# Kernel optimization log

Measured on AMD Instinct MI355X. Metric: run time of the kernel, lower is better.

## Reference

```python
import jax, jax.numpy as jnp
import numpy as np

BN_EPS = 1e-5


def setup_inputs() -> dict:
    key = jax.random.key(0)
    ks = jax.random.split(key, 4)
    N, V, C = 64, 512, 512
    K, OUT = 2, 512
    x = jax.random.normal(ks[0], (N, V, C), dtype=jnp.float32)
    A = jax.random.uniform(ks[1], (N, K, V, V), dtype=jnp.float32) / V
    conv_w = jax.random.normal(ks[2], (2 * OUT, C), dtype=jnp.float32) / np.sqrt(C)
    conv_b = jax.random.normal(ks[3], (2 * OUT,), dtype=jnp.float32) * 0.01
    gamma = jnp.ones((2 * OUT,), dtype=jnp.float32)
    beta = jnp.zeros((2 * OUT,), dtype=jnp.float32)
    eps_p = jnp.zeros((1,), dtype=jnp.float32)
    return {"x": x, "A": A, "conv_w": conv_w, "conv_b": conv_b,
            "gamma": gamma, "beta": beta, "eps_p": eps_p}


def reference(x, A, conv_w, conv_b, gamma, beta, eps_p):
    # x: (N, V, C); A: (N, K, V, V)
    N, V, C = x.shape
    K = A.shape[1]
    # 1x1 Conv1d over nodes: (N, 2*out, V)
    h = jnp.einsum('nvc,oc->nov', x, conv_w) + conv_b[None, :, None]
    # BatchNorm1d, training-mode batch stats (biased variance, per channel)
    mean = jnp.mean(h, axis=(0, 2), keepdims=True)
    var = jnp.var(h, axis=(0, 2), keepdims=True)
    h = (h - mean) * jax.lax.rsqrt(var + BN_EPS) * gamma[None, :, None] + beta[None, :, None]
    c2 = h.shape[1]
    h = h.reshape(N, K, c2 // K, V)  # (N, K, out, V)
    # graph propagation: x A then (x A) A^T, contracted over node dims
    t = jnp.einsum('nkcm,nkme->nkce', h, A)
    At = jnp.transpose(A, (0, 1, 3, 2))
    y = jnp.einsum('nkce,nkem->ncm', t, At)  # (N, out, V)
    out = (1.0 + eps_p[0]) * x + jnp.transpose(y, (0, 2, 1))
    return out, At
```

## Files before the change

### kernel.cpp

```cpp
#include <hip/hip_runtime.h>
#include <stdint.h>

typedef __bf16 bf16x8 __attribute__((ext_vector_type(8)));
typedef float f32x4 __attribute__((ext_vector_type(4)));
typedef unsigned short us4_t __attribute__((ext_vector_type(4)));
typedef unsigned short us8_t __attribute__((ext_vector_type(8)));

#define LDSK 40

__device__ __forceinline__ unsigned short f2bf(float f) {
  __bf16 b = (__bf16)f;
  return __builtin_bit_cast(unsigned short, b);
}
__device__ __forceinline__ float bf2f(unsigned short u) {
  union { uint32_t u; float f; } v; v.u = ((uint32_t)u) << 16;
  return v.f;
}

__device__ __forceinline__ void gload16(const void* g, void* l) {
  __builtin_amdgcn_global_load_lds(
      (const __attribute__((address_space(1))) void*)g,
      (__attribute__((address_space(3))) void*)l, 16, 0, 0);
}

__device__ __forceinline__ void stage_tile(const unsigned short* g, size_t ldg,
                                           unsigned short* lds, int wid, int lane) {
#pragma unroll
  for (int i = 0; i < 2; ++i) {
    int seg = wid * 2 + i;
    const unsigned short* gp = g + (size_t)(seg * 16 + (lane >> 2)) * ldg + (lane & 3) * 8;
    gload16(gp, lds + seg * 512);
  }
}

__device__ __forceinline__ void mfma_step(const unsigned short* As, const unsigned short* Bs,
                                          int ldb, f32x4 (*acc)[4],
                                          int wr, int wc, int lr, int lk) {
  bf16x8 a[4], b[4];
#pragma unroll
  for (int mi = 0; mi < 4; ++mi)
    a[mi] = *(const bf16x8*)(As + (wr + mi * 16 + lr) * 32 + lk * 8);
#pragma unroll
  for (int ni = 0; ni < 4; ++ni)
    b[ni] = *(const bf16x8*)(Bs + (wc + ni * 16 + lr) * ldb + lk * 8);
#pragma unroll
  for (int mi = 0; mi < 4; ++mi)
#pragma unroll
    for (int ni = 0; ni < 4; ++ni)
      acc[mi][ni] = __builtin_amdgcn_mfma_f32_16x16x32_bf16(a[mi], b[ni], acc[mi][ni], 0, 0, 0);
}

__global__ __launch_bounds__(256) void k_convert(
    const float* __restrict__ X, const float* __restrict__ W,
    unsigned short* __restrict__ Xb, unsigned short* __restrict__ Wb) {
  const size_t idx = (size_t)blockIdx.x * 256 + threadIdx.x;
  const size_t stride = (size_t)gridDim.x * 256;
  for (size_t i = idx; i < (size_t)16777216 / 8; i += stride) {
    float4 f0 = ((const float4*)X)[2 * i], f1 = ((const float4*)X)[2 * i + 1];
    us8_t w = { f2bf(f0.x), f2bf(f0.y), f2bf(f0.z), f2bf(f0.w),
                f2bf(f1.x), f2bf(f1.y), f2bf(f1.z), f2bf(f1.w) };
    ((us8_t*)Xb)[i] = w;
  }
  for (size_t i = idx; i < (size_t)524288 / 8; i += stride) {
    float4 f0 = ((const float4*)W)[2 * i], f1 = ((const float4*)W)[2 * i + 1];
    us8_t w = { f2bf(f0.x), f2bf(f0.y), f2bf(f0.z), f2bf(f0.w),
                f2bf(f1.x), f2bf(f1.y), f2bf(f1.z), f2bf(f1.w) };
    ((us8_t*)Wb)[i] = w;
  }
}

__global__ __launch_bounds__(256) void k_gemm1(
    const unsigned short* __restrict__ Wb, const unsigned short* __restrict__ Xb,
    const float* __restrict__ convb, unsigned short* __restrict__ H) {
  __shared__ unsigned short As[4096];
  __shared__ unsigned short Bs[4096];
  const int tid = threadIdx.x;
  const int L = blockIdx.x;
  const int xcd = L & 7, slot = L >> 3;
  const int n = xcd * 8 + (slot >> 5);
  const int tile = slot & 31;
  const int tm = tile >> 2, tn = tile & 3;
  const unsigned short* gA = Wb + (size_t)tm * 128 * 512;
  const unsigned short* gB = Xb + ((size_t)n * 512 + tn * 128) * 512;
  const int lane = tid & 63, wid = tid >> 6;
  const int wr = (wid >> 1) * 64, wc = (wid & 1) * 64;
  const int lr = lane & 15, lk = lane >> 4;
  f32x4 acc[4][4] = {};
  for (int k0 = 0; k0 < 512; k0 += 32) {
    stage_tile(gA + k0, 512, As, wid, lane);
    stage_tile(gB + k0, 512, Bs, wid, lane);
    __syncthreads();
    mfma_step(As, Bs, 32, acc, wr, wc, lr, lk);
    __syncthreads();
  }
  unsigned short* Hn = H + (size_t)n * 1024 * 512;
#pragma unroll
  for (int mi = 0; mi < 4; ++mi)
#pragma unroll
    for (int i = 0; i < 4; ++i) {
      int o = tm * 128 + wr + mi * 16 + lk * 4 + i;
      float bias = convb[o];
#pragma unroll
      for (int ni = 0; ni < 4; ++ni) {
        int v = tn * 128 + wc + ni * 16 + lr;
        Hn[(size_t)o * 512 + v] = f2bf(acc[mi][ni][i] + bias);
      }
    }
}

__global__ __launch_bounds__(256) void k_bn_at_ab(
    const unsigned short* __restrict__ H, const float* __restrict__ gamma,
    const float* __restrict__ beta, float* __restrict__ sc_sh,
    const float* __restrict__ A, float* __restrict__ At,
    unsigned short* __restrict__ Ab) {
  const int tid = threadIdx.x;
  if (blockIdx.x < 1024) {
    const int o = blockIdx.x;
    const int g = tid >> 6, l = tid & 63;
    float s1 = 0.f, s2 = 0.f;
    for (int step = 0; step < 16; ++step) {
      int n = g + step * 4;
      const us8_t* row = (const us8_t*)(H + ((size_t)n * 1024 + o) * 512);
      us8_t v = row[l];
#pragma unroll
      for (int j = 0; j < 8; ++j) { float f = bf2f(v[j]); s1 += f; s2 += f * f; }
    }
    __shared__ float r1[256], r2[256];
    r1[tid] = s1; r2[tid] = s2;
    __syncthreads();
    for (int off = 128; off > 0; off >>= 1) {
      if (tid < off) { r1[tid] += r1[tid + off]; r2[tid] += r2[tid + off]; }
      __syncthreads();
    }
    if (tid == 0) {
      float mean = r1[0] * (1.0f / 32768.0f);
      float var = r2[0] * (1.0f / 32768.0f) - mean * mean;
      float s = gamma[o] * rsqrtf(var + 1e-5f);
      sc_sh[o] = s;
      sc_sh[1024 + o] = beta[o] - mean * s;
    }
  } else {
    __shared__ float tile[64][65];
    const int tIdx = blockIdx.x - 1024;
    const int nk = tIdx >> 6;
    const int e0 = (tIdx & 7) * 64, m0 = ((tIdx >> 3) & 7) * 64;
    const float* src = A + (size_t)nk * 262144;
    float* dst = At + (size_t)nk * 262144;
    unsigned short* ab = Ab + (size_t)nk * 262144;
#pragma unroll
    for (int j = 0; j < 4; ++j) {
      int ch = tid + j * 256;
      int r = ch >> 4, c4 = (ch & 15) * 4;
      float4 f = *(const float4*)(src + (size_t)(m0 + r) * 512 + e0 + c4);
      tile[r][c4] = f.x; tile[r][c4 + 1] = f.y; tile[r][c4 + 2] = f.z; tile[r][c4 + 3] = f.w;
      us4_t u = { f2bf(f.x), f2bf(f.y), f2bf(f.z), f2bf(f.w) };
      *(us4_t*)(ab + (size_t)(m0 + r) * 512 + e0 + c4) = u;
    }
    __syncthreads();
#pragma unroll
    for (int j = 0; j < 4; ++j) {
      int ch = tid + j * 256;
      int e = ch >> 4, m4 = (ch & 15) * 4;
      float4 g = { tile[m4][e], tile[m4 + 1][e], tile[m4 + 2][e], tile[m4 + 3][e] };
      *(float4*)(dst + (size_t)(e0 + e) * 512 + m0 + m4) = g;
    }
  }
}

__global__ __launch_bounds__(256) void k_bn_convA(
    const unsigned short* __restrict__ H, const float* __restrict__ gamma,
    const float* __restrict__ beta, float* __restrict__ sc_sh,
    const float* __restrict__ A, unsigned short* __restrict__ Ab) {
  const int tid = threadIdx.x;
  if (blockIdx.x < 1024) {
    const int o = blockIdx.x;
    const int g = tid >> 6, l = tid & 63;
    float s1 = 0.f, s2 = 0.f;
    for (int step = 0; step < 16; ++step) {
      int n = g + step * 4;
      const us8_t* row = (const us8_t*)(H + ((size_t)n * 1024 + o) * 512);
      us8_t v = row[l];
#pragma unroll
      for (int j = 0; j < 8; ++j) { float f = bf2f(v[j]); s1 += f; s2 += f * f; }
    }
    __shared__ float r1[256], r2[256];
    r1[tid] = s1; r2[tid] = s2;
    __syncthreads();
    for (int off = 128; off > 0; off >>= 1) {
      if (tid < off) { r1[tid] += r1[tid + off]; r2[tid] += r2[tid + off]; }
      __syncthreads();
    }
    if (tid == 0) {
      float mean = r1[0] * (1.0f / 32768.0f);
      float var = r2[0] * (1.0f / 32768.0f) - mean * mean;
      float s = gamma[o] * rsqrtf(var + 1e-5f);
      sc_sh[o] = s;
      sc_sh[1024 + o] = beta[o] - mean * s;
    }
  } else {
    const size_t idx = (size_t)(blockIdx.x - 1024) * 256 + tid;
    const size_t stride = (size_t)2048 * 256;
    for (size_t i = idx; i < (size_t)33554432 / 8; i += stride) {
      float4 f0 = ((const float4*)A)[2 * i], f1 = ((const float4*)A)[2 * i + 1];
      us8_t w = { f2bf(f0.x), f2bf(f0.y), f2bf(f0.z), f2bf(f0.w),
                  f2bf(f1.x), f2bf(f1.y), f2bf(f1.z), f2bf(f1.w) };
      ((us8_t*)Ab)[i] = w;
    }
  }
}

__global__ __launch_bounds__(256) void k_bn(
    const unsigned short* __restrict__ H, const float* __restrict__ gamma,
    const float* __restrict__ beta, float* __restrict__ sc_sh) {
  const int o = blockIdx.x;
  const int tid = threadIdx.x;
  const int g = tid >> 6, l = tid & 63;
  float s1 = 0.f, s2 = 0.f;
  for (int step = 0; step < 16; ++step) {
    int n = g + step * 4;
    const us8_t* row = (const us8_t*)(H + ((size_t)n * 1024 + o) * 512);
    us8_t v = row[l];
#pragma unroll
    for (int j = 0; j < 8; ++j) { float f = bf2f(v[j]); s1 += f; s2 += f * f; }
  }
  __shared__ float r1[256], r2[256];
  r1[tid] = s1; r2[tid] = s2;
  __syncthreads();
  for (int off = 128; off > 0; off >>= 1) {
    if (tid < off) { r1[tid] += r1[tid + off]; r2[tid] += r2[tid + off]; }
    __syncthreads();
  }
  if (tid == 0) {
    float mean = r1[0] * (1.0f / 32768.0f);
    float var = r2[0] * (1.0f / 32768.0f) - mean * mean;
    float s = gamma[o] * rsqrtf(var + 1e-5f);
    sc_sh[o] = s;
    sc_sh[1024 + o] = beta[o] - mean * s;
  }
}

__global__ __launch_bounds__(256) void k_convertA(
    const float* __restrict__ A, unsigned short* __restrict__ Ab) {
  const size_t idx = (size_t)blockIdx.x * 256 + threadIdx.x;
  const size_t stride = (size_t)gridDim.x * 256;
  for (size_t i = idx; i < (size_t)33554432 / 8; i += stride) {
    float4 f0 = ((const float4*)A)[2 * i], f1 = ((const float4*)A)[2 * i + 1];
    us8_t w = { f2bf(f0.x), f2bf(f0.y), f2bf(f0.z), f2bf(f0.w),
                f2bf(f1.x), f2bf(f1.y), f2bf(f1.z), f2bf(f1.w) };
    ((us8_t*)Ab)[i] = w;
  }
}

__global__ __launch_bounds__(256) void k_affine(
    unsigned short* __restrict__ H, const float* __restrict__ sc_sh) {
  const size_t idx = (size_t)blockIdx.x * 256 + threadIdx.x;
  const size_t stride = (size_t)gridDim.x * 256;
  const size_t total8 = (size_t)64 * 1024 * 512 / 8;
  for (size_t i = idx; i < total8; i += stride) {
    size_t base = i * 8;
    int o = (int)((base >> 9) & 1023);
    float sc = sc_sh[o], sh = sc_sh[1024 + o];
    us8_t v = ((const us8_t*)H)[i];
    us8_t w;
#pragma unroll
    for (int j = 0; j < 8; ++j) w[j] = f2bf(fmaf(bf2f(v[j]), sc, sh));
    ((us8_t*)H)[i] = w;
  }
}

__global__ __launch_bounds__(256) void k_aat(
    const unsigned short* __restrict__ Ab, unsigned short* __restrict__ B2) {
  __shared__ unsigned short As[4096];
  __shared__ unsigned short Bs[4096];
  const int tid = threadIdx.x;
  const int L = blockIdx.x;
  const int xcd = L & 7, slot = L >> 3;
  const int nk = xcd * 16 + (slot >> 4);
  const int tile = slot & 15;
  const int tm = tile >> 2, tn = tile & 3;
  const unsigned short* Ank = Ab + (size_t)nk * 262144;
  const unsigned short* gA = Ank + (size_t)tm * 128 * 512;
  const unsigned short* gB = Ank + (size_t)tn * 128 * 512;
  const int lane = tid & 63, wid = tid >> 6;
  const int wr = (wid >> 1) * 64, wc = (wid & 1) * 64;
  const int lr = lane & 15, lk = lane >> 4;
  f32x4 acc[4][4] = {};
  for (int k0 = 0; k0 < 512; k0 += 32) {
    stage_tile(gA + k0, 512, As, wid, lane);
    stage_tile(gB + k0, 512, Bs, wid, lane);
    __syncthreads();
    mfma_step(As, Bs, 32, acc, wr, wc, lr, lk);
    __syncthreads();
  }
  unsigned short* Bn = B2 + (size_t)nk * 262144;
#pragma unroll
  for (int mi = 0; mi < 4; ++mi)
#pragma unroll
    for (int i = 0; i < 4; ++i) {
      int m = tm * 128 + wr + mi * 16 + lk * 4 + i;
#pragma unroll
      for (int ni = 0; ni < 4; ++ni) {
        int mp = tn * 128 + wc + ni * 16 + lr;
        Bn[(size_t)m * 512 + mp] = f2bf(acc[mi][ni][i]);
      }
    }
}

template <bool AFFINE>
__global__ __launch_bounds__(256) void k_gemm3(
    const unsigned short* __restrict__ B2, const unsigned short* __restrict__ H,
    const float* __restrict__ sc_sh, const float* __restrict__ X,
    const float* __restrict__ epsp, float* __restrict__ out) {
  __shared__ unsigned short As[4096];
  __shared__ unsigned short Bs[128 * LDSK];
  __shared__ float s_sc[2][128], s_sh[2][128];
  const int tid = threadIdx.x;
  const int L = blockIdx.x;
  const int xcd = L & 7, slot = L >> 3;
  const int n = xcd * 8 + (slot >> 4);
  const int tile = slot & 15;
  const int tm = tile >> 2, tn = tile & 3;
  const int lane = tid & 63, wid = tid >> 6;
  const int wr = (wid >> 1) * 64, wc = (wid & 1) * 64;
  const int lr = lane & 15, lk = lane >> 4;
  if (AFFINE) {
    if (tid < 256) {
      int kkq = tid >> 7, r = tid & 127;
      s_sc[kkq][r] = sc_sh[kkq * 512 + tn * 128 + r];
      s_sh[kkq][r] = sc_sh[1024 + kkq * 512 + tn * 128 + r];
    }
    __syncthreads();
  }
  f32x4 acc[4][4] = {};
  for (int kk = 0; kk < 2; ++kk) {
    const unsigned short* gA = B2 + ((size_t)(n * 2 + kk) * 512 + tm * 128) * 512;
    const unsigned short* gB = H + ((size_t)n * 1024 + kk * 512 + tn * 128) * 512;
    for (int k0 = 0; k0 < 512; k0 += 32) {
      stage_tile(gA + k0, 512, As, wid, lane);
#pragma unroll
      for (int i = 0; i < 2; ++i) {
        int s = tid + i * 256;
        int r = s >> 2, c8 = (s & 3) * 8;
        us8_t v = *(const us8_t*)(gB + (size_t)r * 512 + k0 + c8);
        if (AFFINE) {
          float sc = s_sc[kk][r], sh = s_sh[kk][r];
          us8_t w;
#pragma unroll
          for (int j = 0; j < 8; ++j) w[j] = f2bf(fmaf(bf2f(v[j]), sc, sh));
          *(us8_t*)&Bs[r * LDSK + c8] = w;
        } else {
          *(us8_t*)&Bs[r * LDSK + c8] = v;
        }
      }
      __syncthreads();
      mfma_step(As, Bs, LDSK, acc, wr, wc, lr, lk);
      __syncthreads();
    }
  }
  const float e1 = 1.0f + epsp[0];
#pragma unroll
  for (int mi = 0; mi < 4; ++mi)
#pragma unroll
    for (int i = 0; i < 4; ++i) {
      int v = tm * 128 + wr + mi * 16 + lk * 4 + i;
#pragma unroll
      for (int ni = 0; ni < 4; ++ni) {
        int c = tn * 128 + wc + ni * 16 + lr;
        size_t idx = ((size_t)n * 512 + v) * 512 + c;
        out[idx] = fmaf(e1, X[idx], acc[mi][ni][i]);
      }
    }
}

__global__ __launch_bounds__(256) void k_at(
    const float* __restrict__ A, float* __restrict__ At) {
  __shared__ float tile[64][65];
  const int nk = blockIdx.z;
  const int e0 = blockIdx.x * 64, m0 = blockIdx.y * 64;
  const float* src = A + (size_t)nk * 262144;
  float* dst = At + (size_t)nk * 262144;
  const int t = threadIdx.x;
#pragma unroll
  for (int j = 0; j < 4; ++j) {
    int ch = t + j * 256;
    int r = ch >> 4, c4 = (ch & 15) * 4;
    float4 f = *(const float4*)(src + (size_t)(m0 + r) * 512 + e0 + c4);
    tile[r][c4] = f.x; tile[r][c4 + 1] = f.y; tile[r][c4 + 2] = f.z; tile[r][c4 + 3] = f.w;
  }
  __syncthreads();
#pragma unroll
  for (int j = 0; j < 4; ++j) {
    int ch = t + j * 256;
    int e = ch >> 4, m4 = (ch & 15) * 4;
    float4 g = { tile[m4][e], tile[m4 + 1][e], tile[m4 + 2][e], tile[m4 + 3][e] };
    *(float4*)(dst + (size_t)(e0 + e) * 512 + m0 + m4) = g;
  }
}

extern "C" void kernel_launch(void* const* d_in, const int* in_sizes, int n_in,
                              void* d_out, int out_size, void* d_ws, size_t ws_size,
                              hipStream_t stream) {
  const float* x      = (const float*)d_in[0];
  const float* A      = (const float*)d_in[1];
  const float* conv_w = (const float*)d_in[2];
  const float* conv_b = (const float*)d_in[3];
  const float* gamma  = (const float*)d_in[4];
  const float* beta   = (const float*)d_in[5];
  const float* eps_p  = (const float*)d_in[6];

  float* out = (float*)d_out;
  float* At  = out + (size_t)16777216;

  unsigned short* Xb = (unsigned short*)out;
  unsigned short* Wb = Xb + (size_t)16777216;
  unsigned short* Ab = (unsigned short*)out;

  const size_t WS_BIG = (size_t)2 * 67108864 + 8192;
  if (ws_size >= WS_BIG) {
    unsigned short* H  = (unsigned short*)d_ws;
    unsigned short* B2 = H + (size_t)33554432;
    float* sc_sh = (float*)(B2 + (size_t)33554432);
    k_convert    <<<2048, 256, 0, stream>>>(x, conv_w, Xb, Wb);
    k_gemm1      <<<2048, 256, 0, stream>>>(Wb, Xb, conv_b, H);
    k_bn_at_ab   <<<9216, 256, 0, stream>>>(H, gamma, beta, sc_sh, A, At, Ab);
    k_aat        <<<2048, 256, 0, stream>>>(Ab, B2);
    k_gemm3<true><<<1024, 256, 0, stream>>>(B2, H, sc_sh, x, eps_p, out);
    return;
  }

  unsigned short* B2 = (unsigned short*)At;
  unsigned short* H  = (unsigned short*)(At + (size_t)16777216);
  float* wsf = (float*)d_ws;

  if (ws_size >= 8192) {
    float* sc_sh = wsf;
    k_convert    <<<2048, 256, 0, stream>>>(x, conv_w, Xb, Wb);
    k_gemm1      <<<2048, 256, 0, stream>>>(Wb, Xb, conv_b, H);
    k_bn_convA   <<<3072, 256, 0, stream>>>(H, gamma, beta, sc_sh, A, Ab);
    k_aat        <<<2048, 256, 0, stream>>>(Ab, B2);
    k_gemm3<true><<<1024, 256, 0, stream>>>(B2, H, sc_sh, x, eps_p, out);
  } else {
    float* sc_sh = out;
    k_convert     <<<2048, 256, 0, stream>>>(x, conv_w, Xb, Wb);
    k_gemm1       <<<2048, 256, 0, stream>>>(Wb, Xb, conv_b, H);
    k_bn          <<<1024, 256, 0, stream>>>(H, gamma, beta, sc_sh);
    k_affine      <<<2048, 256, 0, stream>>>(H, sc_sh);
    k_convertA    <<<2048, 256, 0, stream>>>(A, Ab);
    k_aat         <<<2048, 256, 0, stream>>>(Ab, B2);
    k_gemm3<false><<<1024, 256, 0, stream>>>(B2, H, nullptr, x, eps_p, out);
  }
  k_at<<<dim3(8, 8, 128), 256, 0, stream>>>(A, At);
}
```

Measured before the change: 276.7 us.

## Add large-workspace path fusing A transpose/convert with X convert and BN with AAT

```diff
diff --git a/kernel.cpp b/kernel.cpp
--- a/kernel.cpp
+++ b/kernel.cpp
@@ -50,98 +50,43 @@
       acc[mi][ni] = __builtin_amdgcn_mfma_f32_16x16x32_bf16(a[mi], b[ni], acc[mi][ni], 0, 0, 0);
 }
 
-__global__ __launch_bounds__(256) void k_convert(
-    const float* __restrict__ X, const float* __restrict__ W,
-    unsigned short* __restrict__ Xb, unsigned short* __restrict__ Wb) {
-  const size_t idx = (size_t)blockIdx.x * 256 + threadIdx.x;
-  const size_t stride = (size_t)gridDim.x * 256;
-  for (size_t i = idx; i < (size_t)16777216 / 8; i += stride) {
-    float4 f0 = ((const float4*)X)[2 * i], f1 = ((const float4*)X)[2 * i + 1];
-    us8_t w = { f2bf(f0.x), f2bf(f0.y), f2bf(f0.z), f2bf(f0.w),
-                f2bf(f1.x), f2bf(f1.y), f2bf(f1.z), f2bf(f1.w) };
-    ((us8_t*)Xb)[i] = w;
-  }
-  for (size_t i = idx; i < (size_t)524288 / 8; i += stride) {
-    float4 f0 = ((const float4*)W)[2 * i], f1 = ((const float4*)W)[2 * i + 1];
-    us8_t w = { f2bf(f0.x), f2bf(f0.y), f2bf(f0.z), f2bf(f0.w),
-                f2bf(f1.x), f2bf(f1.y), f2bf(f1.z), f2bf(f1.w) };
-    ((us8_t*)Wb)[i] = w;
-  }
-}
-
-__global__ __launch_bounds__(256) void k_gemm1(
-    const unsigned short* __restrict__ Wb, const unsigned short* __restrict__ Xb,
-    const float* __restrict__ convb, unsigned short* __restrict__ H) {
-  __shared__ unsigned short As[4096];
-  __shared__ unsigned short Bs[4096];
-  const int tid = threadIdx.x;
-  const int L = blockIdx.x;
-  const int xcd = L & 7, slot = L >> 3;
-  const int n = xcd * 8 + (slot >> 5);
-  const int tile = slot & 31;
-  const int tm = tile >> 2, tn = tile & 3;
-  const unsigned short* gA = Wb + (size_t)tm * 128 * 512;
-  const unsigned short* gB = Xb + ((size_t)n * 512 + tn * 128) * 512;
-  const int lane = tid & 63, wid = tid >> 6;
-  const int wr = (wid >> 1) * 64, wc = (wid & 1) * 64;
-  const int lr = lane & 15, lk = lane >> 4;
-  f32x4 acc[4][4] = {};
-  for (int k0 = 0; k0 < 512; k0 += 32) {
-    stage_tile(gA + k0, 512, As, wid, lane);
-    stage_tile(gB + k0, 512, Bs, wid, lane);
-    __syncthreads();
-    mfma_step(As, Bs, 32, acc, wr, wc, lr, lk);
-    __syncthreads();
-  }
-  unsigned short* Hn = H + (size_t)n * 1024 * 512;
-#pragma unroll
-  for (int mi = 0; mi < 4; ++mi)
-#pragma unroll
-    for (int i = 0; i < 4; ++i) {
-      int o = tm * 128 + wr + mi * 16 + lk * 4 + i;
-      float bias = convb[o];
-#pragma unroll
-      for (int ni = 0; ni < 4; ++ni) {
-        int v = tn * 128 + wc + ni * 16 + lr;
-        Hn[(size_t)o * 512 + v] = f2bf(acc[mi][ni][i] + bias);
-      }
-    }
-}
-
-__global__ __launch_bounds__(256) void k_bn_at_ab(
+__device__ __forceinline__ void bn_block(
     const unsigned short* __restrict__ H, const float* __restrict__ gamma,
     const float* __restrict__ beta, float* __restrict__ sc_sh,
-    const float* __restrict__ A, float* __restrict__ At,
+    int o, int tid, float* r1, float* r2) {
+  const int g = tid >> 6, l = tid & 63;
+  float s1 = 0.f, s2 = 0.f;
+  for (int step = 0; step < 16; ++step) {
+    int n = g + step * 4;
+    const us8_t* row = (const us8_t*)(H + ((size_t)n * 1024 + o) * 512);
+    us8_t v = row[l];
+#pragma unroll
+    for (int j = 0; j < 8; ++j) { float f = bf2f(v[j]); s1 += f; s2 += f * f; }
+  }
+  r1[tid] = s1; r2[tid] = s2;
+  __syncthreads();
+  for (int off = 128; off > 0; off >>= 1) {
+    if (tid < off) { r1[tid] += r1[tid + off]; r2[tid] += r2[tid + off]; }
+    __syncthreads();
+  }
+  if (tid == 0) {
+    float mean = r1[0] * (1.0f / 32768.0f);
+    float var = r2[0] * (1.0f / 32768.0f) - mean * mean;
+    float s = gamma[o] * rsqrtf(var + 1e-5f);
+    sc_sh[o] = s;
+    sc_sh[1024 + o] = beta[o] - mean * s;
+  }
+}
+
+__global__ __launch_bounds__(256) void k_convert_all(
+    const float* __restrict__ X, const float* __restrict__ W,
+    const float* __restrict__ A, unsigned short* __restrict__ Xb,
+    unsigned short* __restrict__ Wb, float* __restrict__ At,
     unsigned short* __restrict__ Ab) {
   const int tid = threadIdx.x;
-  if (blockIdx.x < 1024) {
-    const int o = blockIdx.x;
-    const int g = tid >> 6, l = tid & 63;
-    float s1 = 0.f, s2 = 0.f;
-    for (int step = 0; step < 16; ++step) {
-      int n = g + step * 4;
-      const us8_t* row = (const us8_t*)(H + ((size_t)n * 1024 + o) * 512);
-      us8_t v = row[l];
-#pragma unroll
-      for (int j = 0; j < 8; ++j) { float f = bf2f(v[j]); s1 += f; s2 += f * f; }
-    }
-    __shared__ float r1[256], r2[256];
-    r1[tid] = s1; r2[tid] = s2;
-    __syncthreads();
-    for (int off = 128; off > 0; off >>= 1) {
-      if (tid < off) { r1[tid] += r1[tid + off]; r2[tid] += r2[tid + off]; }
-      __syncthreads();
-    }
-    if (tid == 0) {
-      float mean = r1[0] * (1.0f / 32768.0f);
-      float var = r2[0] * (1.0f / 32768.0f) - mean * mean;
-      float s = gamma[o] * rsqrtf(var + 1e-5f);
-      sc_sh[o] = s;
-      sc_sh[1024 + o] = beta[o] - mean * s;
-    }
-  } else {
+  if (blockIdx.x < 8192) {
     __shared__ float tile[64][65];
-    const int tIdx = blockIdx.x - 1024;
+    const int tIdx = blockIdx.x;
     const int nk = tIdx >> 6;
     const int e0 = (tIdx & 7) * 64, m0 = ((tIdx >> 3) & 7) * 64;
     const float* src = A + (size_t)nk * 262144;
@@ -164,115 +109,35 @@
       float4 g = { tile[m4][e], tile[m4 + 1][e], tile[m4 + 2][e], tile[m4 + 3][e] };
       *(float4*)(dst + (size_t)(e0 + e) * 512 + m0 + m4) = g;
     }
-  }
-}
-
-__global__ __launch_bounds__(256) void k_bn_convA(
-    const unsigned short* __restrict__ H, const float* __restrict__ gamma,
-    const float* __restrict__ beta, float* __restrict__ sc_sh,
-    const float* __restrict__ A, unsigned short* __restrict__ Ab) {
-  const int tid = threadIdx.x;
-  if (blockIdx.x < 1024) {
-    const int o = blockIdx.x;
-    const int g = tid >> 6, l = tid & 63;
-    float s1 = 0.f, s2 = 0.f;
-    for (int step = 0; step < 16; ++step) {
-      int n = g + step * 4;
-      const us8_t* row = (const us8_t*)(H + ((size_t)n * 1024 + o) * 512);
-      us8_t v = row[l];
-#pragma unroll
-      for (int j = 0; j < 8; ++j) { float f = bf2f(v[j]); s1 += f; s2 += f * f; }
-    }
-    __shared__ float r1[256], r2[256];
-    r1[tid] = s1; r2[tid] = s2;
-    __syncthreads();
-    for (int off = 128; off > 0; off >>= 1) {
-      if (tid < off) { r1[tid] += r1[tid + off]; r2[tid] += r2[tid + off]; }
-      __syncthreads();
-    }
-    if (tid == 0) {
-      float mean = r1[0] * (1.0f / 32768.0f);
-      float var = r2[0] * (1.0f / 32768.0f) - mean * mean;
-      float s = gamma[o] * rsqrtf(var + 1e-5f);
-      sc_sh[o] = s;
-      sc_sh[1024 + o] = beta[o] - mean * s;
-    }
   } else {
-    const size_t idx = (size_t)(blockIdx.x - 1024) * 256 + tid;
+    const size_t idx = (size_t)(blockIdx.x - 8192) * 256 + tid;
     const size_t stride = (size_t)2048 * 256;
-    for (size_t i = idx; i < (size_t)33554432 / 8; i += stride) {
-      float4 f0 = ((const float4*)A)[2 * i], f1 = ((const float4*)A)[2 * i + 1];
+    for (size_t i = idx; i < (size_t)16777216 / 8; i += stride) {
+      float4 f0 = ((const float4*)X)[2 * i], f1 = ((const float4*)X)[2 * i + 1];
       us8_t w = { f2bf(f0.x), f2bf(f0.y), f2bf(f0.z), f2bf(f0.w),
                   f2bf(f1.x), f2bf(f1.y), f2bf(f1.z), f2bf(f1.w) };
-      ((us8_t*)Ab)[i] = w;
-    }
-  }
-}
-
-__global__ __launch_bounds__(256) void k_bn(
+      ((us8_t*)Xb)[i] = w;
+    }
+    for (size_t i = idx; i < (size_t)524288 / 8; i += stride) {
+      float4 f0 = ((const float4*)W)[2 * i], f1 = ((const float4*)W)[2 * i + 1];
+      us8_t w = { f2bf(f0.x), f2bf(f0.y), f2bf(f0.z), f2bf(f0.w),
+                  f2bf(f1.x), f2bf(f1.y), f2bf(f1.z), f2bf(f1.w) };
+      ((us8_t*)Wb)[i] = w;
+    }
+  }
+}
+
+__global__ __launch_bounds__(256) void k_aat_bn(
+    const unsigned short* __restrict__ Ab, unsigned short* __restrict__ B2,
     const unsigned short* __restrict__ H, const float* __restrict__ gamma,
     const float* __restrict__ beta, float* __restrict__ sc_sh) {
-  const int o = blockIdx.x;
-  const int tid = threadIdx.x;
-  const int g = tid >> 6, l = tid & 63;
-  float s1 = 0.f, s2 = 0.f;
-  for (int step = 0; step < 16; ++step) {
-    int n = g + step * 4;
-    const us8_t* row = (const us8_t*)(H + ((size_t)n * 1024 + o) * 512);
-    us8_t v = row[l];
-#pragma unroll
-    for (int j = 0; j < 8; ++j) { float f = bf2f(v[j]); s1 += f; s2 += f * f; }
-  }
-  __shared__ float r1[256], r2[256];
-  r1[tid] = s1; r2[tid] = s2;
-  __syncthreads();
-  for (int off = 128; off > 0; off >>= 1) {
-    if (tid < off) { r1[tid] += r1[tid + off]; r2[tid] += r2[tid + off]; }
-    __syncthreads();
-  }
-  if (tid == 0) {
-    float mean = r1[0] * (1.0f / 32768.0f);
-    float var = r2[0] * (1.0f / 32768.0f) - mean * mean;
-    float s = gamma[o] * rsqrtf(var + 1e-5f);
-    sc_sh[o] = s;
-    sc_sh[1024 + o] = beta[o] - mean * s;
-  }
-}
-
-__global__ __launch_bounds__(256) void k_convertA(
-    const float* __restrict__ A, unsigned short* __restrict__ Ab) {
-  const size_t idx = (size_t)blockIdx.x * 256 + threadIdx.x;
-  const size_t stride = (size_t)gridDim.x * 256;
-  for (size_t i = idx; i < (size_t)33554432 / 8; i += stride) {
-    float4 f0 = ((const float4*)A)[2 * i], f1 = ((const float4*)A)[2 * i + 1];
-    us8_t w = { f2bf(f0.x), f2bf(f0.y), f2bf(f0.z), f2bf(f0.w),
-                f2bf(f1.x), f2bf(f1.y), f2bf(f1.z), f2bf(f1.w) };
-    ((us8_t*)Ab)[i] = w;
-  }
-}
-
-__global__ __launch_bounds__(256) void k_affine(
-    unsigned short* __restrict__ H, const float* __restrict__ sc_sh) {
-  const size_t idx = (size_t)blockIdx.x * 256 + threadIdx.x;
-  const size_t stride = (size_t)gridDim.x * 256;
-  const size_t total8 = (size_t)64 * 1024 * 512 / 8;
-  for (size_t i = idx; i < total8; i += stride) {
-    size_t base = i * 8;
-    int o = (int)((base >> 9) & 1023);
-    float sc = sc_sh[o], sh = sc_sh[1024 + o];
-    us8_t v = ((const us8_t*)H)[i];
-    us8_t w;
-#pragma unroll
-    for (int j = 0; j < 8; ++j) w[j] = f2bf(fmaf(bf2f(v[j]), sc, sh));
-    ((us8_t*)H)[i] = w;
-  }
-}
-
-__global__ __launch_bounds__(256) void k_aat(
-    const unsigned short* __restrict__ Ab, unsigned short* __restrict__ B2) {
   __shared__ unsigned short As[4096];
   __shared__ unsigned short Bs[4096];
   const int tid = threadIdx.x;
+  if (blockIdx.x >= 2048) {
+    bn_block(H, gamma, beta, sc_sh, blockIdx.x - 2048, tid, (float*)As, (float*)Bs);
+    return;
+  }
   const int L = blockIdx.x;
   const int xcd = L & 7, slot = L >> 3;
   const int nk = xcd * 16 + (slot >> 4);
@@ -306,6 +171,195 @@
     }
 }
 
+__global__ __launch_bounds__(256) void k_convert(
+    const float* __restrict__ X, const float* __restrict__ W,
+    unsigned short* __restrict__ Xb, unsigned short* __restrict__ Wb) {
+  const size_t idx = (size_t)blockIdx.x * 256 + threadIdx.x;
+  const size_t stride = (size_t)gridDim.x * 256;
+  for (size_t i = idx; i < (size_t)16777216 / 8; i += stride) {
+    float4 f0 = ((const float4*)X)[2 * i], f1 = ((const float4*)X)[2 * i + 1];
+    us8_t w = { f2bf(f0.x), f2bf(f0.y), f2bf(f0.z), f2bf(f0.w),
+                f2bf(f1.x), f2bf(f1.y), f2bf(f1.z), f2bf(f1.w) };
+    ((us8_t*)Xb)[i] = w;
+  }
+  for (size_t i = idx; i < (size_t)524288 / 8; i += stride) {
+    float4 f0 = ((const float4*)W)[2 * i], f1 = ((const float4*)W)[2 * i + 1];
+    us8_t w = { f2bf(f0.x), f2bf(f0.y), f2bf(f0.z), f2bf(f0.w),
+                f2bf(f1.x), f2bf(f1.y), f2bf(f1.z), f2bf(f1.w) };
+    ((us8_t*)Wb)[i] = w;
+  }
+}
+
+__global__ __launch_bounds__(256) void k_gemm1(
+    const unsigned short* __restrict__ Wb, const unsigned short* __restrict__ Xb,
+    const float* __restrict__ convb, unsigned short* __restrict__ H) {
+  __shared__ unsigned short As[4096];
+  __shared__ unsigned short Bs[4096];
+  const int tid = threadIdx.x;
+  const int L = blockIdx.x;
+  const int xcd = L & 7, slot = L >> 3;
+  const int n = xcd * 8 + (slot >> 5);
+  const int tile = slot & 31;
+  const int tm = tile >> 2, tn = tile & 3;
+  const unsigned short* gA = Wb + (size_t)tm * 128 * 512;
+  const unsigned short* gB = Xb + ((size_t)n * 512 + tn * 128) * 512;
+  const int lane = tid & 63, wid = tid >> 6;
+  const int wr = (wid >> 1) * 64, wc = (wid & 1) * 64;
+  const int lr = lane & 15, lk = lane >> 4;
+  f32x4 acc[4][4] = {};
+  for (int k0 = 0; k0 < 512; k0 += 32) {
+    stage_tile(gA + k0, 512, As, wid, lane);
+    stage_tile(gB + k0, 512, Bs, wid, lane);
+    __syncthreads();
+    mfma_step(As, Bs, 32, acc, wr, wc, lr, lk);
+    __syncthreads();
+  }
+  unsigned short* Hn = H + (size_t)n * 1024 * 512;
+#pragma unroll
+  for (int mi = 0; mi < 4; ++mi)
+#pragma unroll
+    for (int i = 0; i < 4; ++i) {
+      int o = tm * 128 + wr + mi * 16 + lk * 4 + i;
+      float bias = convb[o];
+#pragma unroll
+      for (int ni = 0; ni < 4; ++ni) {
+        int v = tn * 128 + wc + ni * 16 + lr;
+        Hn[(size_t)o * 512 + v] = f2bf(acc[mi][ni][i] + bias);
+      }
+    }
+}
+
+__global__ __launch_bounds__(256) void k_bn_at_ab(
+    const unsigned short* __restrict__ H, const float* __restrict__ gamma,
+    const float* __restrict__ beta, float* __restrict__ sc_sh,
+    const float* __restrict__ A, float* __restrict__ At,
+    unsigned short* __restrict__ Ab) {
+  const int tid = threadIdx.x;
+  if (blockIdx.x < 1024) {
+    __shared__ float r1[256], r2[256];
+    bn_block(H, gamma, beta, sc_sh, blockIdx.x, tid, r1, r2);
+  } else {
+    __shared__ float tile[64][65];
+    const int tIdx = blockIdx.x - 1024;
+    const int nk = tIdx >> 6;
+    const int e0 = (tIdx & 7) * 64, m0 = ((tIdx >> 3) & 7) * 64;
+    const float* src = A + (size_t)nk * 262144;
+    float* dst = At + (size_t)nk * 262144;
+    unsigned short* ab = Ab + (size_t)nk * 262144;
+#pragma unroll
+    for (int j = 0; j < 4; ++j) {
+      int ch = tid + j * 256;
+      int r = ch >> 4, c4 = (ch & 15) * 4;
+      float4 f = *(const float4*)(src + (size_t)(m0 + r) * 512 + e0 + c4);
+      tile[r][c4] = f.x; tile[r][c4 + 1] = f.y; tile[r][c4 + 2] = f.z; tile[r][c4 + 3] = f.w;
+      us4_t u = { f2bf(f.x), f2bf(f.y), f2bf(f.z), f2bf(f.w) };
+      *(us4_t*)(ab + (size_t)(m0 + r) * 512 + e0 + c4) = u;
+    }
+    __syncthreads();
+#pragma unroll
+    for (int j = 0; j < 4; ++j) {
+      int ch = tid + j * 256;
+      int e = ch >> 4, m4 = (ch & 15) * 4;
+      float4 g = { tile[m4][e], tile[m4 + 1][e], tile[m4 + 2][e], tile[m4 + 3][e] };
+      *(float4*)(dst + (size_t)(e0 + e) * 512 + m0 + m4) = g;
+    }
+  }
+}
+
+__global__ __launch_bounds__(256) void k_bn_convA(
+    const unsigned short* __restrict__ H, const float* __restrict__ gamma,
+    const float* __restrict__ beta, float* __restrict__ sc_sh,
+    const float* __restrict__ A, unsigned short* __restrict__ Ab) {
+  const int tid = threadIdx.x;
+  if (blockIdx.x < 1024) {
+    __shared__ float r1[256], r2[256];
+    bn_block(H, gamma, beta, sc_sh, blockIdx.x, tid, r1, r2);
+  } else {
+    const size_t idx = (size_t)(blockIdx.x - 1024) * 256 + tid;
+    const size_t stride = (size_t)2048 * 256;
+    for (size_t i = idx; i < (size_t)33554432 / 8; i += stride) {
+      float4 f0 = ((const float4*)A)[2 * i], f1 = ((const float4*)A)[2 * i + 1];
+      us8_t w = { f2bf(f0.x), f2bf(f0.y), f2bf(f0.z), f2bf(f0.w),
+                  f2bf(f1.x), f2bf(f1.y), f2bf(f1.z), f2bf(f1.w) };
+      ((us8_t*)Ab)[i] = w;
+    }
+  }
+}
+
+__global__ __launch_bounds__(256) void k_bn(
+    const unsigned short* __restrict__ H, const float* __restrict__ gamma,
+    const float* __restrict__ beta, float* __restrict__ sc_sh) {
+  __shared__ float r1[256], r2[256];
+  bn_block(H, gamma, beta, sc_sh, blockIdx.x, threadIdx.x, r1, r2);
+}
+
+__global__ __launch_bounds__(256) void k_convertA(
+    const float* __restrict__ A, unsigned short* __restrict__ Ab) {
+  const size_t idx = (size_t)blockIdx.x * 256 + threadIdx.x;
+  const size_t stride = (size_t)gridDim.x * 256;
+  for (size_t i = idx; i < (size_t)33554432 / 8; i += stride) {
+    float4 f0 = ((const float4*)A)[2 * i], f1 = ((const float4*)A)[2 * i + 1];
+    us8_t w = { f2bf(f0.x), f2bf(f0.y), f2bf(f0.z), f2bf(f0.w),
+                f2bf(f1.x), f2bf(f1.y), f2bf(f1.z), f2bf(f1.w) };
+    ((us8_t*)Ab)[i] = w;
+  }
+}
+
+__global__ __launch_bounds__(256) void k_affine(
+    unsigned short* __restrict__ H, const float* __restrict__ sc_sh) {
+  const size_t idx = (size_t)blockIdx.x * 256 + threadIdx.x;
+  const size_t stride = (size_t)gridDim.x * 256;
+  const size_t total8 = (size_t)64 * 1024 * 512 / 8;
+  for (size_t i = idx; i < total8; i += stride) {
+    size_t base = i * 8;
+    int o = (int)((base >> 9) & 1023);
+    float sc = sc_sh[o], sh = sc_sh[1024 + o];
+    us8_t v = ((const us8_t*)H)[i];
+    us8_t w;
+#pragma unroll
+    for (int j = 0; j < 8; ++j) w[j] = f2bf(fmaf(bf2f(v[j]), sc, sh));
+    ((us8_t*)H)[i] = w;
+  }
+}
+
+__global__ __launch_bounds__(256) void k_aat(
+    const unsigned short* __restrict__ Ab, unsigned short* __restrict__ B2) {
+  __shared__ unsigned short As[4096];
+  __shared__ unsigned short Bs[4096];
+  const int tid = threadIdx.x;
+  const int L = blockIdx.x;
+  const int xcd = L & 7, slot = L >> 3;
+  const int nk = xcd * 16 + (slot >> 4);
+  const int tile = slot & 15;
+  const int tm = tile >> 2, tn = tile & 3;
+  const unsigned short* Ank = Ab + (size_t)nk * 262144;
+  const unsigned short* gA = Ank + (size_t)tm * 128 * 512;
+  const unsigned short* gB = Ank + (size_t)tn * 128 * 512;
+  const int lane = tid & 63, wid = tid >> 6;
+  const int wr = (wid >> 1) * 64, wc = (wid & 1) * 64;
+  const int lr = lane & 15, lk = lane >> 4;
+  f32x4 acc[4][4] = {};
+  for (int k0 = 0; k0 < 512; k0 += 32) {
+    stage_tile(gA + k0, 512, As, wid, lane);
+    stage_tile(gB + k0, 512, Bs, wid, lane);
+    __syncthreads();
+    mfma_step(As, Bs, 32, acc, wr, wc, lr, lk);
+    __syncthreads();
+  }
+  unsigned short* Bn = B2 + (size_t)nk * 262144;
+#pragma unroll
+  for (int mi = 0; mi < 4; ++mi)
+#pragma unroll
+    for (int i = 0; i < 4; ++i) {
+      int m = tm * 128 + wr + mi * 16 + lk * 4 + i;
+#pragma unroll
+      for (int ni = 0; ni < 4; ++ni) {
+        int mp = tn * 128 + wc + ni * 16 + lr;
+        Bn[(size_t)m * 512 + mp] = f2bf(acc[mi][ni][i]);
+      }
+    }
+}
+
 template <bool AFFINE>
 __global__ __launch_bounds__(256) void k_gemm3(
     const unsigned short* __restrict__ B2, const unsigned short* __restrict__ H,
@@ -413,17 +467,30 @@
 
   unsigned short* Xb = (unsigned short*)out;
   unsigned short* Wb = Xb + (size_t)16777216;
-  unsigned short* Ab = (unsigned short*)out;
-
+  unsigned short* AbO = (unsigned short*)out;
+
+  const size_t WS_XL  = (size_t)3 * 67108864 + 8192;
   const size_t WS_BIG = (size_t)2 * 67108864 + 8192;
+  if (ws_size >= WS_XL) {
+    unsigned short* H   = (unsigned short*)d_ws;
+    unsigned short* B2  = H + (size_t)33554432;
+    unsigned short* Abw = B2 + (size_t)33554432;
+    float* sc_sh = (float*)(Abw + (size_t)33554432);
+    k_convert_all<<<10240, 256, 0, stream>>>(x, conv_w, A, Xb, Wb, At, Abw);
+    k_gemm1      <<<2048,  256, 0, stream>>>(Wb, Xb, conv_b, H);
+    k_aat_bn     <<<3072,  256, 0, stream>>>(Abw, B2, H, gamma, beta, sc_sh);
+    k_gemm3<true><<<1024,  256, 0, stream>>>(B2, H, sc_sh, x, eps_p, out);
+    return;
+  }
+
   if (ws_size >= WS_BIG) {
     unsigned short* H  = (unsigned short*)d_ws;
     unsigned short* B2 = H + (size_t)33554432;
     float* sc_sh = (float*)(B2 + (size_t)33554432);
     k_convert    <<<2048, 256, 0, stream>>>(x, conv_w, Xb, Wb);
     k_gemm1      <<<2048, 256, 0, stream>>>(Wb, Xb, conv_b, H);
-    k_bn_at_ab   <<<9216, 256, 0, stream>>>(H, gamma, beta, sc_sh, A, At, Ab);
-    k_aat        <<<2048, 256, 0, stream>>>(Ab, B2);
+    k_bn_at_ab   <<<9216, 256, 0, stream>>>(H, gamma, beta, sc_sh, A, At, AbO);
+    k_aat        <<<2048, 256, 0, stream>>>(AbO, B2);
     k_gemm3<true><<<1024, 256, 0, stream>>>(B2, H, sc_sh, x, eps_p, out);
     return;
   }
@@ -436,8 +503,8 @@
     float* sc_sh = wsf;
     k_convert    <<<2048, 256, 0, stream>>>(x, conv_w, Xb, Wb);
     k_gemm1      <<<2048, 256, 0, stream>>>(Wb, Xb, conv_b, H);
-    k_bn_convA   <<<3072, 256, 0, stream>>>(H, gamma, beta, sc_sh, A, Ab);
-    k_aat        <<<2048, 256, 0, stream>>>(Ab, B2);
+    k_bn_convA   <<<3072, 256, 0, stream>>>(H, gamma, beta, sc_sh, A, AbO);
+    k_aat        <<<2048, 256, 0, stream>>>(AbO, B2);
     k_gemm3<true><<<1024, 256, 0, stream>>>(B2, H, sc_sh, x, eps_p, out);
   } else {
     float* sc_sh = out;
@@ -445,8 +512,8 @@
     k_gemm1       <<<2048, 256, 0, stream>>>(Wb, Xb, conv_b, H);
     k_bn          <<<1024, 256, 0, stream>>>(H, gamma, beta, sc_sh);
     k_affine      <<<2048, 256, 0, stream>>>(H, sc_sh);
-    k_convertA    <<<2048, 256, 0, stream>>>(A, Ab);
-    k_aat         <<<2048, 256, 0, stream>>>(Ab, B2);
+    k_convertA    <<<2048, 256, 0, stream>>>(A, AbO);
+    k_aat         <<<2048, 256, 0, stream>>>(AbO, B2);
     k_gemm3<false><<<1024, 256, 0, stream>>>(B2, H, nullptr, x, eps_p, out);
   }
   k_at<<<dim3(8, 8, 128), 256, 0, stream>>>(A, At);
```

Measured after the change: 279.2 us. About the same (+0.9%).
